# Performance work log

Hardware: AMD Instinct MI355X
Metric: run time of the kernel (lower is better)

The kernel has to match this reference:

```python
import jax, jax.numpy as jnp
import numpy as np

E, E2, T, C, H = 500_000, 1_000_000, 1_000_000, 64, 64
EPS, EPS2 = 0.0, 0.0  # train_eps=False, eps=eps2=0.0


def setup_inputs() -> dict:
    key = jax.random.key(0)
    ks = jax.random.split(key, 16)
    s = 1.0 / np.sqrt(C)
    return {
        "edge_attr": jax.random.normal(ks[0], (E, C), jnp.float32),
        "edge_attr2": jax.random.normal(ks[1], (E2, C), jnp.float32),
        # 6 projection layers (C -> C)
        "Wp": jax.random.normal(ks[2], (6, C, C), jnp.float32) * s,
        "bp": jnp.zeros((6, C), jnp.float32),
        # MLP 0 (for 1-hop edges): C -> H -> C
        "W1a": jax.random.normal(ks[3], (C, H), jnp.float32) * s,
        "b1a": jnp.zeros((H,), jnp.float32),
        "W2a": jax.random.normal(ks[4], (H, C), jnp.float32) * (1.0 / np.sqrt(H)),
        "b2a": jnp.zeros((C,), jnp.float32),
        # MLP 1 (for 2-hop edges): C -> H -> C
        "W1b": jax.random.normal(ks[5], (C, H), jnp.float32) * s,
        "b1b": jnp.zeros((H,), jnp.float32),
        "W2b": jax.random.normal(ks[6], (H, C), jnp.float32) * (1.0 / np.sqrt(H)),
        "b2b": jnp.zeros((C,), jnp.float32),
        # triangle index lists [3, T]; all values < E so valid for both edge arrays
        "triangle_1_1_1": jax.random.randint(ks[7], (3, T), 0, E, jnp.int64),
        "triangle_1_1_2": jax.random.randint(ks[8], (3, T), 0, E, jnp.int64),
        "triangle_1_2_2": jax.random.randint(ks[9], (3, T), 0, E, jnp.int64),
        "triangle_2_2_2": jax.random.randint(ks[10], (3, T), 0, E, jnp.int64),
        "inverse_edge_1": jax.random.randint(ks[11], (E,), 0, E, jnp.int64),
        "inverse_edge_2": jax.random.randint(ks[12], (E2,), 0, E, jnp.int64),
    }


def reference(edge_attr, edge_attr2, Wp, bp, W1a, b1a, W2a, b2a,
              W1b, b1b, W2b, b2b,
              triangle_1_1_1, triangle_1_1_2, triangle_1_2_2, triangle_2_2_2,
              inverse_edge_1, inverse_edge_2):
    num_edges = edge_attr.shape[0]
    num_edges2 = edge_attr2.shape[0]

    def proj(i, x):  # Linear proj i applied to gathered-sum features
        return x @ Wp[i] + bp[i]

    def mlp_a(x):
        return jax.nn.relu(x @ W1a + b1a) @ W2a + b2a

    def mlp_b(x):
        return jax.nn.relu(x @ W1b + b1b) @ W2b + b2b

    ij111, ik111, kj111 = triangle_1_1_1
    ij112, ik112, kj112 = triangle_1_1_2
    ij122, ik122, kj122 = triangle_1_2_2
    ij222, ik222, kj222 = triangle_2_2_2

    m111 = jax.ops.segment_sum(proj(0, edge_attr[ik111] + edge_attr[kj111]), ij111, num_segments=num_edges)
    m112 = jax.ops.segment_sum(proj(1, edge_attr[ik112] + edge_attr2[kj112]), ij112, num_segments=num_edges)
    m122 = jax.ops.segment_sum(proj(2, edge_attr2[ik122] + edge_attr2[kj122]), ij122, num_segments=num_edges)
    edge_attr = mlp_a(edge_attr * (1.0 + EPS) + m111 + m112 + m112[inverse_edge_1] + m122)

    m211 = jax.ops.segment_sum(proj(3, edge_attr[ij112] + edge_attr[ik112]), kj112, num_segments=num_edges2)
    m212 = jax.ops.segment_sum(proj(4, edge_attr[ij122] + edge_attr2[kj122]), ik122, num_segments=num_edges2)
    m222 = jax.ops.segment_sum(proj(5, edge_attr2[ik222] + edge_attr2[kj222]), ij222, num_segments=num_edges2)
    edge_attr2 = mlp_b(edge_attr2 * (1.0 + EPS2) + m211 + m212 + m212[inverse_edge_2] + m222)

    return (edge_attr, edge_attr2)
```

## Files before the change

kernel.cpp:

```cpp
#include <hip/hip_runtime.h>

#define CH 64
typedef unsigned int uint;
typedef unsigned short ushort;

typedef __attribute__((ext_vector_type(8))) short bf16x8;
typedef __attribute__((ext_vector_type(4))) float f32x4;

__device__ __forceinline__ float bf_lo(uint u){ union{uint a;float f;}c; c.a=u<<16; return c.f; }
__device__ __forceinline__ float bf_hi(uint u){ union{uint a;float f;}c; c.a=u&0xffff0000u; return c.f; }
__device__ __forceinline__ ushort f2bf(float f){
    uint a = __float_as_uint(f);
    a = (a + 0x7fffu + ((a>>16)&1u)) >> 16;
    return (ushort)a;
}
__device__ __forceinline__ uint pack2(float lo, float hi){
    return (uint)f2bf(lo) | ((uint)f2bf(hi) << 16);
}
__device__ __forceinline__ void atom_pk(uint* addr, float lo, float hi){
    uint v = pack2(lo, hi);
    asm volatile("global_atomic_pk_add_bf16 %0, %1, off" :: "v"(addr), "v"(v));
}

struct SJob {
    const void* A; const void* B;
    const int* dst; const int* ia; const int* ib;
    uint* S; float* cnt;
    int T; int abf; int bbf;
};
struct SJobs { SJob j[3]; };

__global__ __launch_bounds__(256) void scatter3_deep(SJobs JJ)
{
    const int nbj = gridDim.x / 3;
    int job = blockIdx.x / nbj; if (job > 2) job = 2;
    const int nb = (job == 2) ? (gridDim.x - 2 * nbj) : nbj;
    const int bj = blockIdx.x - job * nbj;

    const SJob J = JJ.j[job];
    const int l32  = threadIdx.x & 31;
    const int half = (threadIdx.x >> 5) & 1;
    const int wave  = bj * 4 + (threadIdx.x >> 6);
    const int nwave = nb * 4;
    const bool abf = J.abf != 0, bbf = J.bbf != 0;
    const int T = J.T;

    for (int t0 = wave * 8 + half * 4; t0 < T; t0 += nwave * 8) {
        int idd[4], iaa[4], ibb[4]; bool v[4];
        #pragma unroll
        for (int k = 0; k < 4; ++k) {
            const int t = t0 + k;
            v[k] = t < T;
            const int u = v[k] ? t : 0;
            iaa[k] = J.ia[u]; ibb[k] = J.ib[u]; idd[k] = J.dst[u];
        }
        float ax[4], ay[4], bx[4], by[4];
        #pragma unroll
        for (int k = 0; k < 4; ++k) {
            if (abf) { uint u = ((const uint*)J.A)[(size_t)iaa[k]*32 + l32]; ax[k]=bf_lo(u); ay[k]=bf_hi(u); }
            else     { float2 f = ((const float2*)J.A)[(size_t)iaa[k]*32 + l32]; ax[k]=f.x; ay[k]=f.y; }
        }
        #pragma unroll
        for (int k = 0; k < 4; ++k) {
            if (bbf) { uint u = ((const uint*)J.B)[(size_t)ibb[k]*32 + l32]; bx[k]=bf_lo(u); by[k]=bf_hi(u); }
            else     { float2 f = ((const float2*)J.B)[(size_t)ibb[k]*32 + l32]; bx[k]=f.x; by[k]=f.y; }
        }
        #pragma unroll
        for (int k = 0; k < 4; ++k) {
            if (v[k]) {
                atom_pk(J.S + (size_t)idd[k]*32 + l32, ax[k]+bx[k], ay[k]+by[k]);
                if (l32 == 0) atomicAdd(&J.cnt[idd[k]], 1.0f);
            }
        }
    }
}

__global__ __launch_bounds__(256) void conv_bf16_kernel(
    const float* __restrict__ src, uint* __restrict__ dst, long n4)
{
    long i = (long)blockIdx.x * blockDim.x + threadIdx.x;
    const long stride = (long)gridDim.x * blockDim.x;
    for (; i < n4; i += stride) {
        const float4 v = ((const float4*)src)[i];
        uint2 o; o.x = pack2(v.x, v.y); o.y = pack2(v.z, v.w);
        ((uint2*)dst)[i] = o;
    }
}

__global__ __launch_bounds__(256) void fused_finalize_mfma(
    const float* __restrict__ base,
    const uint* __restrict__ SA, const float* __restrict__ cA,
    const float* __restrict__ WA, const float* __restrict__ bA,
    const uint* __restrict__ SB, const float* __restrict__ cB,
    const float* __restrict__ WB, const float* __restrict__ bB,
    const uint* __restrict__ SC, const float* __restrict__ cC,
    const float* __restrict__ WC, const float* __restrict__ bC,
    const int* __restrict__ inv,
    const float* __restrict__ W1, const float* __restrict__ b1,
    const float* __restrict__ W2, const float* __restrict__ b2,
    int N, float* __restrict__ out, uint* __restrict__ out_bf)
{
    __shared__ __attribute__((aligned(16))) char lds[49152];
    const int tid = threadIdx.x;

    const float* Wlist[5] = {WA, WB, WC, W1, W2};
    #pragma unroll
    for (int m = 0; m < 5; ++m) {
        const float* Wm = Wlist[m];
        for (int idx = tid; idx < 4096; idx += 256) {
            const int k = idx >> 6, col = idx & 63;
            *(ushort*)(lds + m*8192 + col*128 + ((2*k) ^ ((col&7)<<4))) = f2bf(Wm[idx]);
        }
    }
    __syncthreads();

    const int w = tid >> 6, lane = tid & 63;
    const int ln = lane & 15, grp = lane >> 4;
    const int r0 = blockIdx.x * 64 + w * 16;
    const int ra = (r0 + ln) < N ? (r0 + ln) : (N - 1);
    const int iva = inv[ra];
    char* zl = lds + 40960 + w * 2048;

    auto ldS = [&](const uint* Srow, int kc) {
        union { uint4 u; bf16x8 h; } c;
        c.u = *(const uint4*)(Srow + kc*16 + grp*4);
        return c.h;
    };
    auto ldS2 = [&](const uint* r1, const uint* r2, int kc) {
        const uint4 a = *(const uint4*)(r1 + kc*16 + grp*4);
        const uint4 b = *(const uint4*)(r2 + kc*16 + grp*4);
        union { uint4 u; bf16x8 h; } c;
        c.u.x = pack2(bf_lo(a.x)+bf_lo(b.x), bf_hi(a.x)+bf_hi(b.x));
        c.u.y = pack2(bf_lo(a.y)+bf_lo(b.y), bf_hi(a.y)+bf_hi(b.y));
        c.u.z = pack2(bf_lo(a.z)+bf_lo(b.z), bf_hi(a.z)+bf_hi(b.z));
        c.u.w = pack2(bf_lo(a.w)+bf_lo(b.w), bf_hi(a.w)+bf_hi(b.w));
        return c.h;
    };
    auto ldW = [&](int m, int kc, int ct) {
        const int col = ct*16 + ln;
        const int k2  = (kc*32 + grp*8) * 2;
        return *(const bf16x8*)(lds + m*8192 + col*128 + (k2 ^ ((col&7)<<4)));
    };
    auto ldZ = [&](int kc) {
        const int k2 = (kc*32 + grp*8) * 2;
        return *(const bf16x8*)(zl + ln*128 + (k2 ^ ((ln&7)<<4)));
    };
    auto stZ = [&](int row, int col, float v) {
        *(ushort*)(zl + row*128 + ((2*col) ^ ((row&7)<<4))) = f2bf(v);
    };

    const uint* SArow  = SA + (size_t)ra * 32;
    const uint* SBrow  = SB + (size_t)ra * 32;
    const uint* SCrow  = SC + (size_t)ra * 32;
    const uint* SCrow2 = SC + (size_t)iva * 32;

    const f32x4 z4 = {0.f, 0.f, 0.f, 0.f};
    f32x4 acc[4] = {z4, z4, z4, z4};

    #pragma unroll
    for (int kc = 0; kc < 2; ++kc) {
        const bf16x8 aA = ldS(SArow, kc);
        const bf16x8 aB = ldS(SBrow, kc);
        const bf16x8 aC = ldS2(SCrow, SCrow2, kc);
        #pragma unroll
        for (int ct = 0; ct < 4; ++ct) {
            acc[ct] = __builtin_amdgcn_mfma_f32_16x16x32_bf16(aA, ldW(0,kc,ct), acc[ct], 0,0,0);
            acc[ct] = __builtin_amdgcn_mfma_f32_16x16x32_bf16(aB, ldW(1,kc,ct), acc[ct], 0,0,0);
            acc[ct] = __builtin_amdgcn_mfma_f32_16x16x32_bf16(aC, ldW(2,kc,ct), acc[ct], 0,0,0);
        }
    }

    #pragma unroll
    for (int reg = 0; reg < 4; ++reg) {
        const int rd = r0 + grp*4 + reg;
        const int rc = rd < N ? rd : (N - 1);
        const float fA = cA[rc], fB = cB[rc];
        const float fC = cC[rc] + cC[inv[rc]];
        #pragma unroll
        for (int ct = 0; ct < 4; ++ct) {
            const int col = ct*16 + ln;
            acc[ct][reg] += base[(size_t)rc*64 + col] + fA*bA[col] + fB*bB[col] + fC*bC[col];
        }
    }
    #pragma unroll
    for (int ct = 0; ct < 4; ++ct)
        #pragma unroll
        for (int reg = 0; reg < 4; ++reg)
            stZ(grp*4 + reg, ct*16 + ln, acc[ct][reg]);

    f32x4 hacc[4] = {z4, z4, z4, z4};
    #pragma unroll
    for (int kc = 0; kc < 2; ++kc) {
        const bf16x8 az = ldZ(kc);
        #pragma unroll
        for (int ct = 0; ct < 4; ++ct)
            hacc[ct] = __builtin_amdgcn_mfma_f32_16x16x32_bf16(az, ldW(3,kc,ct), hacc[ct], 0,0,0);
    }
    #pragma unroll
    for (int ct = 0; ct < 4; ++ct)
        #pragma unroll
        for (int reg = 0; reg < 4; ++reg)
            stZ(grp*4 + reg, ct*16 + ln, fmaxf(hacc[ct][reg] + b1[ct*16 + ln], 0.f));

    f32x4 oacc[4] = {z4, z4, z4, z4};
    #pragma unroll
    for (int kc = 0; kc < 2; ++kc) {
        const bf16x8 ah = ldZ(kc);
        #pragma unroll
        for (int ct = 0; ct < 4; ++ct)
            oacc[ct] = __builtin_amdgcn_mfma_f32_16x16x32_bf16(ah, ldW(4,kc,ct), oacc[ct], 0,0,0);
    }
    #pragma unroll
    for (int reg = 0; reg < 4; ++reg) {
        const int rd = r0 + grp*4 + reg;
        if (rd < N) {
            #pragma unroll
            for (int ct = 0; ct < 4; ++ct) {
                const int col = ct*16 + ln;
                const float o = oacc[ct][reg] + b2[col];
                out[(size_t)rd*64 + col] = o;
                if (out_bf) ((ushort*)out_bf)[(size_t)rd*64 + col] = f2bf(o);
            }
        }
    }
}

extern "C" void kernel_launch(void* const* d_in, const int* in_sizes, int n_in,
                              void* d_out, int out_size, void* d_ws, size_t ws_size,
                              hipStream_t stream)
{
    const float* ea  = (const float*)d_in[0];
    const float* ea2 = (const float*)d_in[1];
    const float* Wp  = (const float*)d_in[2];
    const float* bp  = (const float*)d_in[3];
    const float* W1a = (const float*)d_in[4];
    const float* b1a = (const float*)d_in[5];
    const float* W2a = (const float*)d_in[6];
    const float* b2a = (const float*)d_in[7];
    const float* W1b = (const float*)d_in[8];
    const float* b1b = (const float*)d_in[9];
    const float* W2b = (const float*)d_in[10];
    const float* b2b = (const float*)d_in[11];
    const int* t111 = (const int*)d_in[12];
    const int* t112 = (const int*)d_in[13];
    const int* t122 = (const int*)d_in[14];
    const int* t222 = (const int*)d_in[15];
    const int* inv1 = (const int*)d_in[16];
    const int* inv2 = (const int*)d_in[17];

    const int E    = in_sizes[0] / CH;
    const int E2   = in_sizes[1] / CH;
    const int T111 = in_sizes[12] / 3;
    const int T112 = in_sizes[13] / 3;
    const int T122 = in_sizes[14] / 3;
    const int T222 = in_sizes[15] / 3;

    float* out1 = (float*)d_out;
    float* out2 = out1 + (size_t)E * CH;

    const size_t R = (size_t)(E > E2 ? E : E2);
    char* p = (char*)d_ws;
    uint*  Sbase = (uint*)p;  p += 3 * R * 128;
    float* cbase = (float*)p; p += 3 * R * 4;
    size_t used = (size_t)(p - (char*)d_ws);
    uint* ea2_bf = nullptr;
    uint* out1_bf = nullptr;
    uint* ea_bf  = nullptr;
    if (ws_size >= used + (size_t)E2 * 128) { ea2_bf = (uint*)p; p += (size_t)E2 * 128; used += (size_t)E2 * 128; }
    if (ws_size >= used + (size_t)E  * 128) { out1_bf = (uint*)p; p += (size_t)E * 128; used += (size_t)E * 128; }
    if (ws_size >= used + (size_t)E  * 128) { ea_bf  = (uint*)p; }

    const dim3 blk256(256);
    const int SCAT_NB = 4096;

    if (ea2_bf) conv_bf16_kernel<<<2048, blk256, 0, stream>>>(ea2, ea2_bf, (long)E2 * 16);
    if (ea_bf)  conv_bf16_kernel<<<2048, blk256, 0, stream>>>(ea,  ea_bf,  (long)E  * 16);

    const void* eaS  = ea_bf  ? (const void*)ea_bf  : (const void*)ea;
    const void* ea2S = ea2_bf ? (const void*)ea2_bf : (const void*)ea2;
    const int eaB = ea_bf != nullptr, ea2B = ea2_bf != nullptr;

    uint*  SA1 = Sbase;              uint*  SB1 = Sbase + (size_t)E * 32;  uint*  SC1 = Sbase + (size_t)2*E * 32;
    float* cA1 = cbase;              float* cB1 = cbase + E;               float* cC1 = cbase + (size_t)2*E;
    hipMemsetAsync(Sbase, 0, (size_t)3 * E * 128, stream);
    hipMemsetAsync(cbase, 0, (size_t)3 * E * 4, stream);

    {
        SJobs J;
        J.j[0] = {eaS,  eaS,  t111 + 0, t111 + T111, t111 + 2*T111, SA1, cA1, T111, eaB,  eaB};
        J.j[1] = {ea2S, ea2S, t122 + 0, t122 + T122, t122 + 2*T122, SB1, cB1, T122, ea2B, ea2B};
        J.j[2] = {eaS,  ea2S, t112 + 0, t112 + T112, t112 + 2*T112, SC1, cC1, T112, eaB,  ea2B};
        scatter3_deep<<<SCAT_NB, blk256, 0, stream>>>(J);
    }

    fused_finalize_mfma<<<(E + 63) / 64, blk256, 0, stream>>>(
        ea,
        SA1, cA1, Wp + 0*CH*CH, bp + 0*CH,
        SB1, cB1, Wp + 2*CH*CH, bp + 2*CH,
        SC1, cC1, Wp + 1*CH*CH, bp + 1*CH,
        inv1, W1a, b1a, W2a, b2a, E, out1, out1_bf);

    uint*  SA2 = Sbase;              uint*  SB2 = Sbase + (size_t)E2 * 32; uint*  SC2 = Sbase + (size_t)2*E2 * 32;
    float* cA2 = cbase;              float* cB2 = cbase + E2;              float* cC2 = cbase + (size_t)2*E2;
    hipMemsetAsync(Sbase, 0, (size_t)3 * E2 * 128, stream);
    hipMemsetAsync(cbase, 0, (size_t)3 * E2 * 4, stream);

    const void* o1S = out1_bf ? (const void*)out1_bf : (const void*)out1;
    const int o1B = out1_bf != nullptr;

    {
        SJobs J;
        J.j[0] = {o1S,  o1S,  t112 + 2*T112, t112 + 0, t112 + T112,   SA2, cA2, T112, o1B,  o1B};
        J.j[1] = {ea2S, ea2S, t222 + 0,      t222 + T222, t222 + 2*T222, SB2, cB2, T222, ea2B, ea2B};
        J.j[2] = {o1S,  ea2S, t122 + T122,   t122 + 0, t122 + 2*T122, SC2, cC2, T122, o1B,  ea2B};
        scatter3_deep<<<SCAT_NB, blk256, 0, stream>>>(J);
    }

    fused_finalize_mfma<<<(E2 + 63) / 64, blk256, 0, stream>>>(
        ea2,
        SA2, cA2, Wp + 3*CH*CH, bp + 3*CH,
        SB2, cB2, Wp + 5*CH*CH, bp + 5*CH,
        SC2, cC2, Wp + 4*CH*CH, bp + 4*CH,
        inv2, W1b, b1b, W2b, b2b, E2, out2, nullptr);
}
```

Before: 1.604 ms.

## Replace atomic bf16 scatter with CSR build and per-row gather reduction

Replaces the scatter kernel, which did packed-bf16 atomic adds into the message buffers, with a destination-sorted CSR. A histogram, a three-kernel prefix scan and an atomic-cursor fill build it, then one half-wave per destination row gathers and sums its triangles in fp32 and writes the row once. The aim is to remove the wide random atomic read-modify-write traffic and the memsets of the message buffers. It also accumulates in fp32 before a single bf16 rounding. The cost is several extra launches, extra passes over the index arrays, int atomics for the histogram and fill, and a chain of dependent loads (csr, then index, then feature row) inside a serial per-row loop.

```diff
diff --git a/kernel.cpp b/kernel.cpp
--- a/kernel.cpp
+++ b/kernel.cpp
@@ -17,61 +17,113 @@
 __device__ __forceinline__ uint pack2(float lo, float hi){
     return (uint)f2bf(lo) | ((uint)f2bf(hi) << 16);
 }
-__device__ __forceinline__ void atom_pk(uint* addr, float lo, float hi){
-    uint v = pack2(lo, hi);
-    asm volatile("global_atomic_pk_add_bf16 %0, %1, off" :: "v"(addr), "v"(v));
-}
-
-struct SJob {
+
+struct GJob {
     const void* A; const void* B;
     const int* dst; const int* ia; const int* ib;
-    uint* S; float* cnt;
+    uint* S;
+    int* cnt;
+    const int* offs;
+    int* cursor;
     int T; int abf; int bbf;
 };
-struct SJobs { SJob j[3]; };
-
-__global__ __launch_bounds__(256) void scatter3_deep(SJobs JJ)
+struct GJobs { GJob j[3]; int E; };
+
+__global__ __launch_bounds__(256) void hist3(GJobs G)
 {
     const int nbj = gridDim.x / 3;
     int job = blockIdx.x / nbj; if (job > 2) job = 2;
-    const int nb = (job == 2) ? (gridDim.x - 2 * nbj) : nbj;
+    const int nb = (job == 2) ? (gridDim.x - 2*nbj) : nbj;
     const int bj = blockIdx.x - job * nbj;
-
-    const SJob J = JJ.j[job];
-    const int l32  = threadIdx.x & 31;
-    const int half = (threadIdx.x >> 5) & 1;
-    const int wave  = bj * 4 + (threadIdx.x >> 6);
-    const int nwave = nb * 4;
+    const GJob J = G.j[job];
+    for (int t = bj*256 + threadIdx.x; t < J.T; t += nb*256)
+        atomicAdd(&J.cnt[J.dst[t]], 1);
+}
+
+#define SCHUNK 2048
+__global__ __launch_bounds__(256) void scan_a(const int* __restrict__ cnt, int n, int* __restrict__ bsum)
+{
+    __shared__ int l[256];
+    const int tid = threadIdx.x;
+    const int base = blockIdx.x * SCHUNK + tid * 8;
+    int s = 0;
+    #pragma unroll
+    for (int i = 0; i < 8; ++i) { const int idx = base + i; s += (idx < n) ? cnt[idx] : 0; }
+    l[tid] = s; __syncthreads();
+    if (tid == 0) { int tot = 0; for (int i = 0; i < 256; ++i) tot += l[i]; bsum[blockIdx.x] = tot; }
+}
+__global__ __launch_bounds__(256) void scan_b(int* __restrict__ bsum, int nb)
+{
+    __shared__ int l[256];
+    const int tid = threadIdx.x;
+    const int chunk = (nb + 255) / 256;
+    const int lo = tid * chunk, hi = (tid+1)*chunk < nb ? (tid+1)*chunk : nb;
+    int s = 0;
+    for (int i = lo; i < hi; ++i) s += bsum[i];
+    l[tid] = s; __syncthreads();
+    if (tid == 0) { int run = 0; for (int i = 0; i < 256; ++i) { int v = l[i]; l[i] = run; run += v; } }
+    __syncthreads();
+    int run = l[tid];
+    for (int i = lo; i < hi; ++i) { int v = bsum[i]; bsum[i] = run; run += v; }
+}
+__global__ __launch_bounds__(256) void scan_c(const int* __restrict__ cnt, int n,
+                                              const int* __restrict__ bsum, int* __restrict__ offs)
+{
+    __shared__ int l[256];
+    const int tid = threadIdx.x;
+    const int base = blockIdx.x * SCHUNK + tid * 8;
+    int v[8]; int s = 0;
+    #pragma unroll
+    for (int i = 0; i < 8; ++i) { const int idx = base + i; v[i] = (idx < n) ? cnt[idx] : 0; s += v[i]; }
+    l[tid] = s; __syncthreads();
+    if (tid == 0) { int run = 0; for (int i = 0; i < 256; ++i) { int x = l[i]; l[i] = run; run += x; } }
+    __syncthreads();
+    int run = bsum[blockIdx.x] + l[tid];
+    #pragma unroll
+    for (int i = 0; i < 8; ++i) { const int idx = base + i; if (idx < n) offs[idx] = run; run += v[i]; }
+}
+
+__global__ __launch_bounds__(256) void fill3(GJobs G, int* __restrict__ csr)
+{
+    const int nbj = gridDim.x / 3;
+    int job = blockIdx.x / nbj; if (job > 2) job = 2;
+    const int nb = (job == 2) ? (gridDim.x - 2*nbj) : nbj;
+    const int bj = blockIdx.x - job * nbj;
+    const GJob J = G.j[job];
+    for (int t = bj*256 + threadIdx.x; t < J.T; t += nb*256) {
+        const int d = J.dst[t];
+        const int pos = atomicAdd(&J.cursor[d], 1);
+        csr[pos] = t;
+    }
+}
+
+__global__ __launch_bounds__(256) void gather3(GJobs G, const int* __restrict__ csr)
+{
+    const int nbj = gridDim.x / 3;
+    int job = blockIdx.x / nbj; if (job > 2) job = 2;
+    const int nb = (job == 2) ? (gridDim.x - 2*nbj) : nbj;
+    const int bj = blockIdx.x - job * nbj;
+    const GJob J = G.j[job];
+    const int l32 = threadIdx.x & 31;
+    const int hw  = ((bj << 8) + threadIdx.x) >> 5;
+    const int nhw = (nb << 8) >> 5;
     const bool abf = J.abf != 0, bbf = J.bbf != 0;
-    const int T = J.T;
-
-    for (int t0 = wave * 8 + half * 4; t0 < T; t0 += nwave * 8) {
-        int idd[4], iaa[4], ibb[4]; bool v[4];
-        #pragma unroll
-        for (int k = 0; k < 4; ++k) {
-            const int t = t0 + k;
-            v[k] = t < T;
-            const int u = v[k] ? t : 0;
-            iaa[k] = J.ia[u]; ibb[k] = J.ib[u]; idd[k] = J.dst[u];
-        }
-        float ax[4], ay[4], bx[4], by[4];
-        #pragma unroll
-        for (int k = 0; k < 4; ++k) {
-            if (abf) { uint u = ((const uint*)J.A)[(size_t)iaa[k]*32 + l32]; ax[k]=bf_lo(u); ay[k]=bf_hi(u); }
-            else     { float2 f = ((const float2*)J.A)[(size_t)iaa[k]*32 + l32]; ax[k]=f.x; ay[k]=f.y; }
-        }
-        #pragma unroll
-        for (int k = 0; k < 4; ++k) {
-            if (bbf) { uint u = ((const uint*)J.B)[(size_t)ibb[k]*32 + l32]; bx[k]=bf_lo(u); by[k]=bf_hi(u); }
-            else     { float2 f = ((const float2*)J.B)[(size_t)ibb[k]*32 + l32]; bx[k]=f.x; by[k]=f.y; }
-        }
-        #pragma unroll
-        for (int k = 0; k < 4; ++k) {
-            if (v[k]) {
-                atom_pk(J.S + (size_t)idd[k]*32 + l32, ax[k]+bx[k], ay[k]+by[k]);
-                if (l32 == 0) atomicAdd(&J.cnt[idd[k]], 1.0f);
-            }
-        }
+    const int E = G.E;
+
+    for (int r = hw; r < E; r += nhw) {
+        const int n    = J.cnt[r];
+        const int base = J.offs[r];
+        float a0 = 0.f, a1 = 0.f;
+        for (int k = 0; k < n; ++k) {
+            const int t  = csr[base + k];
+            const int ia = J.ia[t];
+            const int ib = J.ib[t];
+            if (abf) { const uint u = ((const uint*)J.A)[(size_t)ia*32 + l32]; a0 += bf_lo(u); a1 += bf_hi(u); }
+            else     { const float2 f = ((const float2*)J.A)[(size_t)ia*32 + l32]; a0 += f.x; a1 += f.y; }
+            if (bbf) { const uint u = ((const uint*)J.B)[(size_t)ib*32 + l32]; a0 += bf_lo(u); a1 += bf_hi(u); }
+            else     { const float2 f = ((const float2*)J.B)[(size_t)ib*32 + l32]; a0 += f.x; a1 += f.y; }
+        }
+        J.S[(size_t)r*32 + l32] = pack2(a0, a1);
     }
 }
 
@@ -89,11 +141,11 @@
 
 __global__ __launch_bounds__(256) void fused_finalize_mfma(
     const float* __restrict__ base,
-    const uint* __restrict__ SA, const float* __restrict__ cA,
+    const uint* __restrict__ SA, const int* __restrict__ cA,
     const float* __restrict__ WA, const float* __restrict__ bA,
-    const uint* __restrict__ SB, const float* __restrict__ cB,
+    const uint* __restrict__ SB, const int* __restrict__ cB,
     const float* __restrict__ WB, const float* __restrict__ bB,
-    const uint* __restrict__ SC, const float* __restrict__ cC,
+    const uint* __restrict__ SC, const int* __restrict__ cC,
     const float* __restrict__ WC, const float* __restrict__ bC,
     const int* __restrict__ inv,
     const float* __restrict__ W1, const float* __restrict__ b1,
@@ -174,8 +226,8 @@
     for (int reg = 0; reg < 4; ++reg) {
         const int rd = r0 + grp*4 + reg;
         const int rc = rd < N ? rd : (N - 1);
-        const float fA = cA[rc], fB = cB[rc];
-        const float fC = cC[rc] + cC[inv[rc]];
+        const float fA = (float)cA[rc], fB = (float)cB[rc];
+        const float fC = (float)(cC[rc] + cC[inv[rc]]);
         #pragma unroll
         for (int ct = 0; ct < 4; ++ct) {
             const int col = ct*16 + ln;
@@ -259,9 +311,17 @@
     float* out2 = out1 + (size_t)E * CH;
 
     const size_t R = (size_t)(E > E2 ? E : E2);
+    const int Tsum1 = T111 + T122 + T112;
+    const int Tsum2 = T112 + T222 + T122;
+    const int Tcap  = Tsum1 > Tsum2 ? Tsum1 : Tsum2;
+
     char* p = (char*)d_ws;
-    uint*  Sbase = (uint*)p;  p += 3 * R * 128;
-    float* cbase = (float*)p; p += 3 * R * 4;
+    uint*  Sbase  = (uint*)p;  p += 3 * R * 128;
+    int*   cntI   = (int*)p;   p += 3 * R * 4;
+    int*   offs   = (int*)p;   p += 3 * R * 4;
+    int*   cursor = (int*)p;   p += 3 * R * 4;
+    int*   csr    = (int*)p;   p += (size_t)Tcap * 4;
+    int*   bsum   = (int*)p;   p += 8192 * 4;
     size_t used = (size_t)(p - (char*)d_ws);
     uint* ea2_bf = nullptr;
     uint* out1_bf = nullptr;
@@ -271,7 +331,7 @@
     if (ws_size >= used + (size_t)E  * 128) { ea_bf  = (uint*)p; }
 
     const dim3 blk256(256);
-    const int SCAT_NB = 4096;
+    const int NB3 = 3072;
 
     if (ea2_bf) conv_bf16_kernel<<<2048, blk256, 0, stream>>>(ea2, ea2_bf, (long)E2 * 16);
     if (ea_bf)  conv_bf16_kernel<<<2048, blk256, 0, stream>>>(ea,  ea_bf,  (long)E  * 16);
@@ -280,46 +340,50 @@
     const void* ea2S = ea2_bf ? (const void*)ea2_bf : (const void*)ea2;
     const int eaB = ea_bf != nullptr, ea2B = ea2_bf != nullptr;
 
-    uint*  SA1 = Sbase;              uint*  SB1 = Sbase + (size_t)E * 32;  uint*  SC1 = Sbase + (size_t)2*E * 32;
-    float* cA1 = cbase;              float* cB1 = cbase + E;               float* cC1 = cbase + (size_t)2*E;
-    hipMemsetAsync(Sbase, 0, (size_t)3 * E * 128, stream);
-    hipMemsetAsync(cbase, 0, (size_t)3 * E * 4, stream);
-
+    auto run_phase = [&](GJobs& G, int Eph) {
+        const int n3 = 3 * Eph;
+        const int nbs = (n3 + SCHUNK - 1) / SCHUNK;
+        hipMemsetAsync(cntI, 0, (size_t)n3 * 4, stream);
+        hist3<<<NB3, blk256, 0, stream>>>(G);
+        scan_a<<<nbs, blk256, 0, stream>>>(cntI, n3, bsum);
+        scan_b<<<1,   blk256, 0, stream>>>(bsum, nbs);
+        scan_c<<<nbs, blk256, 0, stream>>>(cntI, n3, bsum, offs);
+        hipMemcpyAsync(cursor, offs, (size_t)n3 * 4, hipMemcpyDeviceToDevice, stream);
+        fill3<<<NB3, blk256, 0, stream>>>(G, csr);
+        gather3<<<NB3, blk256, 0, stream>>>(G, csr);
+    };
+
+    uint*  SA1 = Sbase;           uint*  SB1 = Sbase + (size_t)E*32;  uint*  SC1 = Sbase + (size_t)2*E*32;
     {
-        SJobs J;
-        J.j[0] = {eaS,  eaS,  t111 + 0, t111 + T111, t111 + 2*T111, SA1, cA1, T111, eaB,  eaB};
-        J.j[1] = {ea2S, ea2S, t122 + 0, t122 + T122, t122 + 2*T122, SB1, cB1, T122, ea2B, ea2B};
-        J.j[2] = {eaS,  ea2S, t112 + 0, t112 + T112, t112 + 2*T112, SC1, cC1, T112, eaB,  ea2B};
-        scatter3_deep<<<SCAT_NB, blk256, 0, stream>>>(J);
+        GJobs G; G.E = E;
+        G.j[0] = {eaS,  eaS,  t111 + 0, t111 + T111, t111 + 2*T111, SA1, cntI,       offs,       cursor,       T111, eaB,  eaB};
+        G.j[1] = {ea2S, ea2S, t122 + 0, t122 + T122, t122 + 2*T122, SB1, cntI + E,   offs + E,   cursor + E,   T122, ea2B, ea2B};
+        G.j[2] = {eaS,  ea2S, t112 + 0, t112 + T112, t112 + 2*T112, SC1, cntI + 2*E, offs + 2*E, cursor + 2*E, T112, eaB,  ea2B};
+        run_phase(G, E);
     }
 
     fused_finalize_mfma<<<(E + 63) / 64, blk256, 0, stream>>>(
         ea,
-        SA1, cA1, Wp + 0*CH*CH, bp + 0*CH,
-        SB1, cB1, Wp + 2*CH*CH, bp + 2*CH,
-        SC1, cC1, Wp + 1*CH*CH, bp + 1*CH,
+        SA1, cntI,       Wp + 0*CH*CH, bp + 0*CH,
+        SB1, cntI + E,   Wp + 2*CH*CH, bp + 2*CH,
+        SC1, cntI + 2*E, Wp + 1*CH*CH, bp + 1*CH,
         inv1, W1a, b1a, W2a, b2a, E, out1, out1_bf);
 
-    uint*  SA2 = Sbase;              uint*  SB2 = Sbase + (size_t)E2 * 32; uint*  SC2 = Sbase + (size_t)2*E2 * 32;
-    float* cA2 = cbase;              float* cB2 = cbase + E2;              float* cC2 = cbase + (size_t)2*E2;
-    hipMemsetAsync(Sbase, 0, (size_t)3 * E2 * 128, stream);
-    hipMemsetAsync(cbase, 0, (size_t)3 * E2 * 4, stream);
-
+    uint*  SA2 = Sbase;           uint*  SB2 = Sbase + (size_t)E2*32; uint*  SC2 = Sbase + (size_t)2*E2*32;
     const void* o1S = out1_bf ? (const void*)out1_bf : (const void*)out1;
     const int o1B = out1_bf != nullptr;
-
     {
-        SJobs J;
-        J.j[0] = {o1S,  o1S,  t112 + 2*T112, t112 + 0, t112 + T112,   SA2, cA2, T112, o1B,  o1B};
-        J.j[1] = {ea2S, ea2S, t222 + 0,      t222 + T222, t222 + 2*T222, SB2, cB2, T222, ea2B, ea2B};
-        J.j[2] = {o1S,  ea2S, t122 + T122,   t122 + 0, t122 + 2*T122, SC2, cC2, T122, o1B,  ea2B};
-        scatter3_deep<<<SCAT_NB, blk256, 0, stream>>>(J);
+        GJobs G; G.E = E2;
+        G.j[0] = {o1S,  o1S,  t112 + 2*T112, t112 + 0,    t112 + T112,   SA2, cntI,        offs,        cursor,        T112, o1B,  o1B};
+        G.j[1] = {ea2S, ea2S, t222 + 0,      t222 + T222, t222 + 2*T222, SB2, cntI + E2,   offs + E2,   cursor + E2,   T222, ea2B, ea2B};
+        G.j[2] = {o1S,  ea2S, t122 + T122,   t122 + 0,    t122 + 2*T122, SC2, cntI + 2*E2, offs + 2*E2, cursor + 2*E2, T122, o1B,  ea2B};
+        run_phase(G, E2);
     }
 
     fused_finalize_mfma<<<(E2 + 63) / 64, blk256, 0, stream>>>(
         ea2,
-        SA2, cA2, Wp + 3*CH*CH, bp + 3*CH,
-        SB2, cB2, Wp + 5*CH*CH, bp + 5*CH,
-        SC2, cC2, Wp + 4*CH*CH, bp + 4*CH,
+        SA2, cntI,        Wp + 3*CH*CH, bp + 3*CH,
+        SB2, cntI + E2,   Wp + 5*CH*CH, bp + 5*CH,
+        SC2, cntI + 2*E2, Wp + 4*CH*CH, bp + 4*CH,
         inv2, W1b, b1b, W2b, b2b, E2, out2, nullptr);
 }
```

New measurement: 2.713 ms. 1.69x slower.
